# Optimization experiments

Hardware: AMD Instinct MI355X
Metric: run time of the kernel (lower is better)

## Reference

```python
import jax, jax.numpy as jnp
import numpy as np

N_NODES = 100000
N_EDGES = 1000000
N_GRAPHS = 2000
D = 64
BN_EPS = 1e-5


def setup_inputs() -> dict:
    key = jax.random.key(0)
    ks = jax.random.split(key, 16)
    x = jax.random.normal(ks[0], (N_NODES, D), dtype=jnp.float32)
    edge_index = jax.random.randint(ks[1], (2, N_EDGES), 0, N_NODES, dtype=jnp.int64)
    batch = jnp.sort(jax.random.randint(ks[2], (N_NODES,), 0, N_GRAPHS, dtype=jnp.int64))
    convW = jax.random.normal(ks[3], (3, D, D), dtype=jnp.float32) * 0.1
    convb = jax.random.normal(ks[4], (3, D), dtype=jnp.float32) * 0.1
    bn_gamma = jax.random.uniform(ks[5], (3, D), dtype=jnp.float32) + 0.5
    bn_beta = jax.random.normal(ks[6], (3, D), dtype=jnp.float32) * 0.1
    bn_mean = jax.random.normal(ks[7], (3, D), dtype=jnp.float32) * 0.1
    bn_var = jax.random.uniform(ks[8], (3, D), dtype=jnp.float32) + 0.5
    eps = jnp.zeros((3,), dtype=jnp.float32)
    clfW0 = jax.random.normal(ks[9], (256, 256), dtype=jnp.float32) * 0.05
    clfb0 = jax.random.normal(ks[10], (256,), dtype=jnp.float32) * 0.05
    clfW1 = jax.random.normal(ks[11], (256, 128), dtype=jnp.float32) * 0.05
    clfb1 = jax.random.normal(ks[12], (128,), dtype=jnp.float32) * 0.05
    finalW = jax.random.normal(ks[13], (128, 1), dtype=jnp.float32) * 0.05
    finalb = jnp.zeros((1,), dtype=jnp.float32)
    return {"x": x, "edge_index": edge_index, "batch": batch, "convW": convW,
            "convb": convb, "bn_gamma": bn_gamma, "bn_beta": bn_beta,
            "bn_mean": bn_mean, "bn_var": bn_var, "eps": eps,
            "clfW0": clfW0, "clfb0": clfb0, "clfW1": clfW1, "clfb1": clfb1,
            "finalW": finalW, "finalb": finalb}


def reference(x, edge_index, batch, convW, convb, bn_gamma, bn_beta, bn_mean,
              bn_var, eps, clfW0, clfb0, clfW1, clfb1, finalW, finalb):
    leaky = jax.nn.leaky_relu  # slope 0.01, matches torch default
    src, dst = edge_index[0], edge_index[1]
    n = x.shape[0]
    hs = []
    for l in range(3):
        # GINConv: (1 + eps) * x_i + sum_{j in N(i)} x_j  (scatter-add over edges)
        agg = jax.ops.segment_sum(x[src], dst, num_segments=n)
        h = (1.0 + eps[l]) * x + agg
        # MLP: Linear -> BatchNorm1d (eval, running stats) -> LeakyReLU (Dropout is identity in eval)
        h = h @ convW[l] + convb[l]
        h = (h - bn_mean[l]) * jax.lax.rsqrt(bn_var[l] + BN_EPS) * bn_gamma[l] + bn_beta[l]
        h = leaky(h)
        # extra LeakyReLU applied in GIN.forward after each conv layer
        h = leaky(h)
        x = h
        hs.append(h)
    # global_add_pool then repeat_interleave back to nodes (batch is sorted)
    h_pool = jax.ops.segment_sum(x, batch, num_segments=N_GRAPHS)
    h_pool_per_node = h_pool[batch]
    h = jnp.concatenate(hs + [h_pool_per_node], axis=1)  # [N, 256]
    h = leaky(h @ clfW0 + clfb0)
    h = leaky(h @ clfW1 + clfb1)
    h = h @ finalW + finalb
    return jax.nn.sigmoid(h)
```

## Files before the change

### kernel.cpp

```cpp
#include <hip/hip_runtime.h>

#define N_NODES 100000
#define PADM    100096
#define N_EDGES 1000000
#define N_GRAPHS 2000
#define D 64

typedef __bf16    bf16x8 __attribute__((ext_vector_type(8)));
typedef __bf16    bf16x4 __attribute__((ext_vector_type(4)));
typedef float     f32x4  __attribute__((ext_vector_type(4)));

__device__ __forceinline__ size_t apack(int row, int col, int fpr) {
  int frag = (row >> 4) * fpr + (col >> 5);
  int lane = (((col & 31) >> 3) << 4) | (row & 15);
  return (size_t)frag * 512 + lane * 8 + (col & 7);
}

__global__ __launch_bounds__(256) void deg_hist_kernel(
    const int* __restrict__ ei, int* __restrict__ deg)
{
  int i = blockIdx.x * blockDim.x + threadIdx.x;
  if (i < N_EDGES) atomicAdd(&deg[ei[N_EDGES + i]], 1);
}

__global__ __launch_bounds__(256) void scan1_kernel(
    const int* __restrict__ deg, int* __restrict__ incl, int* __restrict__ bsum)
{
  __shared__ int sh[256];
  int t = threadIdx.x;
  int base = blockIdx.x * 2048 + t * 8;
  int v[8];
  int run = 0;
#pragma unroll
  for (int j = 0; j < 8; ++j) {
    int idx = base + j;
    int xv = (idx < N_NODES) ? deg[idx] : 0;
    run += xv;
    v[j] = run;
  }
  sh[t] = run;
  __syncthreads();
  for (int off = 1; off < 256; off <<= 1) {
    int a = (t >= off) ? sh[t - off] : 0;
    __syncthreads();
    sh[t] += a;
    __syncthreads();
  }
  int prev = (t > 0) ? sh[t - 1] : 0;
#pragma unroll
  for (int j = 0; j < 8; ++j) {
    int idx = base + j;
    if (idx < N_NODES) incl[idx] = v[j] + prev;
  }
  if (t == 255) bsum[blockIdx.x] = sh[255];
}

__global__ void scan2_kernel(int* __restrict__ bsum, int nb)
{
  if (blockIdx.x == 0 && threadIdx.x == 0) {
    int run = 0;
    for (int i = 0; i < nb; ++i) { int xv = bsum[i]; bsum[i] = run; run += xv; }
  }
}

__global__ __launch_bounds__(256) void scan3_kernel(
    const int* __restrict__ incl, const int* __restrict__ bsum,
    const int* __restrict__ deg, int* __restrict__ row_ptr, int* __restrict__ cursor)
{
  int i = blockIdx.x * blockDim.x + threadIdx.x;
  if (i < N_NODES) {
    int val = incl[i] + bsum[i >> 11];
    row_ptr[i + 1] = val;
    cursor[i] = val - deg[i];
    if (i == 0) row_ptr[0] = 0;
  }
}

__global__ __launch_bounds__(256) void fill_csr_kernel(
    const int* __restrict__ ei, int* __restrict__ cursor, int* __restrict__ srcs)
{
  int i = blockIdx.x * blockDim.x + threadIdx.x;
  if (i < N_EDGES) {
    int s = ei[i];
    int d = ei[N_EDGES + i];
    int pos = atomicAdd(&cursor[d], 1);
    srcs[pos] = s;
  }
}

__global__ __launch_bounds__(256) void split_x_kernel(
    const float* __restrict__ x, __bf16* __restrict__ xhi, __bf16* __restrict__ xlo)
{
  int idx = blockIdx.x * blockDim.x + threadIdx.x;
  if (idx >= N_NODES * 16) return;
  int v = idx >> 4, c4 = (idx & 15) << 2;
  float4 xv = *(const float4*)(x + (size_t)v * D + c4);
  float p[4] = {xv.x, xv.y, xv.z, xv.w};
  bf16x4 vh, vl;
#pragma unroll
  for (int j = 0; j < 4; ++j) {
    __bf16 h = (__bf16)p[j];
    vh[j] = h;
    vl[j] = (__bf16)(p[j] - (float)h);
  }
  size_t o = apack(v, c4, 2);
  *(bf16x4*)(xhi + o) = vh;
  *(bf16x4*)(xlo + o) = vl;
}

__global__ __launch_bounds__(256) void wconv_kernel(
    const float* __restrict__ W0, const float* __restrict__ W1,
    const float* __restrict__ convW,
    __bf16* __restrict__ w0hi, __bf16* __restrict__ w0lo,
    __bf16* __restrict__ w1hi, __bf16* __restrict__ w1lo,
    __bf16* __restrict__ cwhi, __bf16* __restrict__ cwlo)
{
  int i = blockIdx.x * 256 + threadIdx.x;
  if (i < 65536) {
    int k = i >> 8, n = i & 255;
    float v = W0[i];
    __bf16 h = (__bf16)v;
    size_t o = apack(n, k, 8);
    w0hi[o] = h;
    w0lo[o] = (__bf16)(v - (float)h);
  }
  if (i < 32768) {
    int k = i >> 7, n = i & 127;
    float v = W1[i];
    __bf16 h = (__bf16)v;
    size_t o = apack(n, k, 8);
    w1hi[o] = h;
    w1lo[o] = (__bf16)(v - (float)h);
  }
  if (i < 12288) {
    int l = i >> 12, rem = i & 4095;
    int k = rem >> 6, n = rem & 63;
    float v = convW[i];
    __bf16 h = (__bf16)v;
    size_t o = (size_t)l * 4096 + apack(n, k, 2);
    cwhi[o] = h;
    cwlo[o] = (__bf16)(v - (float)h);
  }
}

__global__ __launch_bounds__(256) void ygemm_kernel(
    const __bf16* __restrict__ Ahi, const __bf16* __restrict__ Alo,
    int fpr, int fbase,
    const __bf16* __restrict__ cwh, const __bf16* __restrict__ cwl,
    float* __restrict__ y)
{
  int t = threadIdx.x;
  int wid = t >> 6, lane = t & 63;
  int bm0 = blockIdx.x * 64 + wid * 16;
  int rowtile = bm0 >> 4;
  int l15 = lane & 15;
  f32x4 acc[4];
#pragma unroll
  for (int j = 0; j < 4; ++j) acc[j] = (f32x4){0.f, 0.f, 0.f, 0.f};

#pragma unroll
  for (int kc = 0; kc < 2; ++kc) {
    bf16x8 ah, al, bh[4], bl[4];
    {
      size_t off = (size_t)(rowtile * fpr + fbase + kc) * 512 + lane * 8;
      ah = *(const bf16x8*)(Ahi + off);
      al = *(const bf16x8*)(Alo + off);
    }
#pragma unroll
    for (int ct = 0; ct < 4; ++ct) {
      size_t off = (size_t)(ct * 2 + kc) * 512 + lane * 8;
      bh[ct] = *(const bf16x8*)(cwh + off);
      bl[ct] = *(const bf16x8*)(cwl + off);
    }
#pragma unroll
    for (int ct = 0; ct < 4; ++ct) {
      acc[ct] = __builtin_amdgcn_mfma_f32_16x16x32_bf16(ah, bh[ct], acc[ct], 0, 0, 0);
      acc[ct] = __builtin_amdgcn_mfma_f32_16x16x32_bf16(al, bh[ct], acc[ct], 0, 0, 0);
      acc[ct] = __builtin_amdgcn_mfma_f32_16x16x32_bf16(ah, bl[ct], acc[ct], 0, 0, 0);
      acc[ct] = __builtin_amdgcn_mfma_f32_16x16x32_bf16(al, bl[ct], acc[ct], 0, 0, 0);
    }
  }
  int rbase = (lane >> 4) * 4;
#pragma unroll
  for (int ct = 0; ct < 4; ++ct)
#pragma unroll
    for (int r = 0; r < 4; ++r)
      y[(size_t)(bm0 + rbase + r) * D + 16 * ct + l15] = acc[ct][r];
}

template <int POOL>
__global__ __launch_bounds__(256) void agg_bn_kernel(
    const float* __restrict__ y,
    const int* __restrict__ row_ptr, const int* __restrict__ srcs,
    const float* __restrict__ bias,
    const float* __restrict__ gamma, const float* __restrict__ beta,
    const float* __restrict__ mean, const float* __restrict__ var,
    const float* __restrict__ epsp,
    __bf16* __restrict__ ohi, __bf16* __restrict__ olo, int oc0,
    float* __restrict__ hpool, const int* __restrict__ batch)
{
  int wid = (blockIdx.x * blockDim.x + threadIdx.x) >> 6;
  int lane = threadIdx.x & 63;
  if (wid >= N_NODES) return;
  float onepe = 1.0f + epsp[0];
  int beg = row_ptr[wid];
  int end = row_ptr[wid + 1];
  float s = onepe * y[(size_t)wid * D + lane];
  int e = beg;
  for (; e + 8 <= end; e += 8) {
    int i0 = srcs[e], i1 = srcs[e + 1], i2 = srcs[e + 2], i3 = srcs[e + 3];
    int i4 = srcs[e + 4], i5 = srcs[e + 5], i6 = srcs[e + 6], i7 = srcs[e + 7];
    float a0 = y[(size_t)i0 * D + lane];
    float a1 = y[(size_t)i1 * D + lane];
    float a2 = y[(size_t)i2 * D + lane];
    float a3 = y[(size_t)i3 * D + lane];
    float a4 = y[(size_t)i4 * D + lane];
    float a5 = y[(size_t)i5 * D + lane];
    float a6 = y[(size_t)i6 * D + lane];
    float a7 = y[(size_t)i7 * D + lane];
    s += ((a0 + a1) + (a2 + a3)) + ((a4 + a5) + (a6 + a7));
  }
  for (; e + 4 <= end; e += 4) {
    int i0 = srcs[e], i1 = srcs[e + 1], i2 = srcs[e + 2], i3 = srcs[e + 3];
    float a0 = y[(size_t)i0 * D + lane];
    float a1 = y[(size_t)i1 * D + lane];
    float a2 = y[(size_t)i2 * D + lane];
    float a3 = y[(size_t)i3 * D + lane];
    s += (a0 + a1) + (a2 + a3);
  }
  for (; e < end; ++e) s += y[(size_t)srcs[e] * D + lane];

  float sc = gamma[lane] * rsqrtf(var[lane] + 1e-5f);
  float z = (s + bias[lane] - mean[lane]) * sc + beta[lane];
  z = (z > 0.f) ? z : 0.01f * z;
  z = (z > 0.f) ? z : 0.01f * z;
  __bf16 h = (__bf16)z;
  size_t o = apack(wid, oc0 + lane, 8);
  ohi[o] = h;
  olo[o] = (__bf16)(z - (float)h);
  if (POOL) {
    int g = batch[wid];
    unsafeAtomicAdd(&hpool[(size_t)g * D + lane], z);
  }
}

__global__ __launch_bounds__(256) void pool_expand_kernel(
    const float* __restrict__ hpool, const int* __restrict__ batch,
    __bf16* __restrict__ ohi, __bf16* __restrict__ olo)
{
  int idx = blockIdx.x * blockDim.x + threadIdx.x;
  int v = idx >> 4, c4 = (idx & 15) << 2;
  if (v >= N_NODES) return;
  int g = batch[v];
  float4 pv = *(const float4*)(hpool + (size_t)g * D + c4);
  float p[4] = {pv.x, pv.y, pv.z, pv.w};
  bf16x4 vh, vl;
#pragma unroll
  for (int j = 0; j < 4; ++j) {
    __bf16 h = (__bf16)p[j];
    vh[j] = h;
    vl[j] = (__bf16)(p[j] - (float)h);
  }
  size_t o = apack(v, 192 + c4, 8);
  *(bf16x4*)(ohi + o) = vh;
  *(bf16x4*)(olo + o) = vl;
}

__global__ __launch_bounds__(256) void clf_fused_kernel(
    const __bf16* __restrict__ Ahi, const __bf16* __restrict__ Alo,
    const __bf16* __restrict__ w0h, const __bf16* __restrict__ w0l,
    const float* __restrict__ b0,
    const __bf16* __restrict__ w1h, const __bf16* __restrict__ w1l,
    const float* __restrict__ b1,
    const float* __restrict__ Wf, const float* __restrict__ fbias,
    float* __restrict__ out)
{
  __shared__ __bf16 HaS[64 * 128];
  __shared__ __bf16 LaS[64 * 128];
  int t = threadIdx.x;
  int w = t >> 6, lane = t & 63;
  int wr = w >> 1, wc = w & 1;
  int l15 = lane & 15, g = lane >> 4, lk = g * 8;
  int bm0 = blockIdx.x * 64;
  int rtile0 = (bm0 >> 4) + 2 * wr;

  f32x4 acc2[2][4];
#pragma unroll
  for (int i = 0; i < 2; ++i)
#pragma unroll
    for (int j = 0; j < 4; ++j) acc2[i][j] = (f32x4){0.f, 0.f, 0.f, 0.f};

  for (int h = 0; h < 2; ++h) {
    f32x4 acc[2][4];
#pragma unroll
    for (int i = 0; i < 2; ++i)
#pragma unroll
      for (int j = 0; j < 4; ++j) acc[i][j] = (f32x4){0.f, 0.f, 0.f, 0.f};

    int ntile0 = 8 * h + 4 * wc;
    for (int ks = 0; ks < 8; ++ks) {
      bf16x8 ah[2], al[2], bh[4], bl[4];
#pragma unroll
      for (int rt = 0; rt < 2; ++rt) {
        size_t off = (size_t)((rtile0 + rt) * 8 + ks) * 512 + lane * 8;
        ah[rt] = *(const bf16x8*)(Ahi + off);
        al[rt] = *(const bf16x8*)(Alo + off);
      }
#pragma unroll
      for (int ct = 0; ct < 4; ++ct) {
        size_t off = (size_t)((ntile0 + ct) * 8 + ks) * 512 + lane * 8;
        bh[ct] = *(const bf16x8*)(w0h + off);
        bl[ct] = *(const bf16x8*)(w0l + off);
      }
#pragma unroll
      for (int rt = 0; rt < 2; ++rt)
#pragma unroll
        for (int ct = 0; ct < 4; ++ct) {
          acc[rt][ct] = __builtin_amdgcn_mfma_f32_16x16x32_bf16(ah[rt], bh[ct], acc[rt][ct], 0, 0, 0);
          acc[rt][ct] = __builtin_amdgcn_mfma_f32_16x16x32_bf16(al[rt], bh[ct], acc[rt][ct], 0, 0, 0);
          acc[rt][ct] = __builtin_amdgcn_mfma_f32_16x16x32_bf16(ah[rt], bl[ct], acc[rt][ct], 0, 0, 0);
        }
    }
#pragma unroll
    for (int rt = 0; rt < 2; ++rt)
#pragma unroll
      for (int ct = 0; ct < 4; ++ct) {
        int coll = 64 * wc + 16 * ct + l15;
        float bb = b0[128 * h + coll];
#pragma unroll
        for (int r = 0; r < 4; ++r) {
          int rowl = 32 * wr + 16 * rt + 4 * g + r;
          float z = acc[rt][ct][r] + bb;
          z = (z > 0.f) ? z : 0.01f * z;
          __bf16 hv = (__bf16)z;
          unsigned bo = (unsigned)(rowl * 256 + coll * 2) ^ ((rowl & 7) << 4);
          *(__bf16*)((char*)HaS + bo) = hv;
          *(__bf16*)((char*)LaS + bo) = (__bf16)(z - (float)hv);
        }
      }
    __syncthreads();

    for (int ks = 0; ks < 4; ++ks) {
      int kl = ks * 32;
      bf16x8 ah2[2], al2[2], b2h[4], b2l[4];
#pragma unroll
      for (int rt = 0; rt < 2; ++rt) {
        int rowl = 32 * wr + 16 * rt + l15;
        unsigned bo = (unsigned)(rowl * 256 + (kl + lk) * 2) ^ ((rowl & 7) << 4);
        ah2[rt] = *(const bf16x8*)((char*)HaS + bo);
        al2[rt] = *(const bf16x8*)((char*)LaS + bo);
      }
#pragma unroll
      for (int ct = 0; ct < 4; ++ct) {
        size_t off = (size_t)((4 * wc + ct) * 8 + 4 * h + ks) * 512 + lane * 8;
        b2h[ct] = *(const bf16x8*)(w1h + off);
        b2l[ct] = *(const bf16x8*)(w1l + off);
      }
#pragma unroll
      for (int rt = 0; rt < 2; ++rt)
#pragma unroll
        for (int ct = 0; ct < 4; ++ct) {
          acc2[rt][ct] = __builtin_amdgcn_mfma_f32_16x16x32_bf16(ah2[rt], b2h[ct], acc2[rt][ct], 0, 0, 0);
          acc2[rt][ct] = __builtin_amdgcn_mfma_f32_16x16x32_bf16(al2[rt], b2h[ct], acc2[rt][ct], 0, 0, 0);
          acc2[rt][ct] = __builtin_amdgcn_mfma_f32_16x16x32_bf16(ah2[rt], b2l[ct], acc2[rt][ct], 0, 0, 0);
        }
    }
    __syncthreads();
  }

  float* partS = (float*)HaS;
#pragma unroll
  for (int rt = 0; rt < 2; ++rt) {
#pragma unroll
    for (int r = 0; r < 4; ++r) {
      int rowl = 32 * wr + 16 * rt + 4 * g + r;
      float p = 0.f;
#pragma unroll
      for (int ct = 0; ct < 4; ++ct) {
        int c = 64 * wc + 16 * ct + l15;
        float z = acc2[rt][ct][r] + b1[c];
        z = (z > 0.f) ? z : 0.01f * z;
        p += z * Wf[c];
      }
      p += __shfl_xor(p, 1);
      p += __shfl_xor(p, 2);
      p += __shfl_xor(p, 4);
      p += __shfl_xor(p, 8);
      if (l15 == 0) partS[wc * 64 + rowl] = p;
    }
  }
  __syncthreads();
  if (t < 64) {
    int gl = bm0 + t;
    if (gl < N_NODES) {
      float z = partS[t] + partS[64 + t] + fbias[0];
      out[gl] = 1.0f / (1.0f + expf(-z));
    }
  }
}

extern "C" void kernel_launch(void* const* d_in, const int* in_sizes, int n_in,
                              void* d_out, int out_size, void* d_ws, size_t ws_size,
                              hipStream_t stream)
{
  const float* x     = (const float*)d_in[0];
  const int*   ei    = (const int*)d_in[1];
  const int*   batch = (const int*)d_in[2];
  const float* convW = (const float*)d_in[3];
  const float* convb = (const float*)d_in[4];
  const float* gam   = (const float*)d_in[5];
  const float* bet   = (const float*)d_in[6];
  const float* mean  = (const float*)d_in[7];
  const float* var   = (const float*)d_in[8];
  const float* eps   = (const float*)d_in[9];
  const float* W0    = (const float*)d_in[10];
  const float* b0    = (const float*)d_in[11];
  const float* W1    = (const float*)d_in[12];
  const float* b1    = (const float*)d_in[13];
  const float* Wf    = (const float*)d_in[14];
  const float* fb    = (const float*)d_in[15];
  float* out = (float*)d_out;

  float* ws = (float*)d_ws;
  __bf16* A0hi = (__bf16*)(ws);
  __bf16* A0lo = (__bf16*)(ws + 12812288);
  float*  y    = ws + 25624576;
  __bf16* xhi  = (__bf16*)(ws + 32030720);
  __bf16* xlo  = (__bf16*)(ws + 35230720);
  int* deg     = (int*)(ws + 38436864);
  int* incl    = (int*)(ws + 38536864);
  int* row_ptr = (int*)(ws + 38636864);
  int* cursor  = (int*)(ws + 38736896);
  int* srcs    = (int*)(ws + 38836896);
  int* bsum    = (int*)(ws + 39836896);
  float* hpool = ws + 39836960;
  __bf16* w0hi = (__bf16*)(ws + 39964960);
  __bf16* w0lo = (__bf16*)(ws + 39997728);
  __bf16* w1hi = (__bf16*)(ws + 40030496);
  __bf16* w1lo = (__bf16*)(ws + 40046880);
  __bf16* cwhi = (__bf16*)(ws + 40063264);
  __bf16* cwlo = (__bf16*)(ws + 40069408);

  dim3 b256(256);

  wconv_kernel<<<256, b256, 0, stream>>>(W0, W1, convW, w0hi, w0lo, w1hi, w1lo, cwhi, cwlo);

  hipMemsetAsync(deg, 0, (size_t)N_NODES * sizeof(int), stream);
  deg_hist_kernel<<<(N_EDGES + 255) / 256, b256, 0, stream>>>(ei, deg);
  scan1_kernel<<<(N_NODES + 2047) / 2048, b256, 0, stream>>>(deg, incl, bsum);
  scan2_kernel<<<1, 64, 0, stream>>>(bsum, (N_NODES + 2047) / 2048);
  scan3_kernel<<<(N_NODES + 255) / 256, b256, 0, stream>>>(incl, bsum, deg, row_ptr, cursor);
  fill_csr_kernel<<<(N_EDGES + 255) / 256, b256, 0, stream>>>(ei, cursor, srcs);

  hipMemsetAsync(hpool, 0, (size_t)N_GRAPHS * D * sizeof(float), stream);
  split_x_kernel<<<(N_NODES * 16 + 255) / 256, b256, 0, stream>>>(x, xhi, xlo);

  int ygrid = PADM / 64;
  int aggGrid = (N_NODES * 64 + 255) / 256;

  ygemm_kernel<<<ygrid, b256, 0, stream>>>(xhi, xlo, 2, 0, cwhi, cwlo, y);
  agg_bn_kernel<0><<<aggGrid, b256, 0, stream>>>(
      y, row_ptr, srcs, convb, gam, bet, mean, var, eps, A0hi, A0lo, 0, nullptr, nullptr);
  ygemm_kernel<<<ygrid, b256, 0, stream>>>(A0hi, A0lo, 8, 0, cwhi + 4096, cwlo + 4096, y);
  agg_bn_kernel<0><<<aggGrid, b256, 0, stream>>>(
      y, row_ptr, srcs, convb + D, gam + D, bet + D, mean + D, var + D, eps + 1,
      A0hi, A0lo, 64, nullptr, nullptr);
  ygemm_kernel<<<ygrid, b256, 0, stream>>>(A0hi, A0lo, 8, 2, cwhi + 8192, cwlo + 8192, y);
  agg_bn_kernel<1><<<aggGrid, b256, 0, stream>>>(
      y, row_ptr, srcs, convb + 2 * D, gam + 2 * D, bet + 2 * D, mean + 2 * D,
      var + 2 * D, eps + 2, A0hi, A0lo, 128, hpool, batch);

  pool_expand_kernel<<<(N_NODES * 16 + 255) / 256, b256, 0, stream>>>(hpool, batch, A0hi, A0lo);

  clf_fused_kernel<<<PADM / 64, b256, 0, stream>>>(
      A0hi, A0lo, w0hi, w0lo, b0, w1hi, w1lo, b1, Wf, fb, out);
}
```

Measured before the change: 438.3 us.

## Process four nodes per wave with float4 gathers in aggregation kernel

```diff
diff --git a/kernel.cpp b/kernel.cpp
--- a/kernel.cpp
+++ b/kernel.cpp
@@ -199,48 +199,67 @@
     __bf16* __restrict__ ohi, __bf16* __restrict__ olo, int oc0,
     float* __restrict__ hpool, const int* __restrict__ batch)
 {
-  int wid = (blockIdx.x * blockDim.x + threadIdx.x) >> 6;
+  int wave = (blockIdx.x * blockDim.x + threadIdx.x) >> 6;
   int lane = threadIdx.x & 63;
-  if (wid >= N_NODES) return;
+  int sub = lane >> 4;
+  int sl  = lane & 15;
+  int node = wave * 4 + sub;
+  if (node >= N_NODES) return;
   float onepe = 1.0f + epsp[0];
-  int beg = row_ptr[wid];
-  int end = row_ptr[wid + 1];
-  float s = onepe * y[(size_t)wid * D + lane];
+  int beg = row_ptr[node];
+  int end = row_ptr[node + 1];
+  const float4* yv = (const float4*)y;
+  float4 own = yv[(size_t)node * 16 + sl];
+  float4 s = make_float4(onepe * own.x, onepe * own.y, onepe * own.z, onepe * own.w);
   int e = beg;
-  for (; e + 8 <= end; e += 8) {
-    int i0 = srcs[e], i1 = srcs[e + 1], i2 = srcs[e + 2], i3 = srcs[e + 3];
-    int i4 = srcs[e + 4], i5 = srcs[e + 5], i6 = srcs[e + 6], i7 = srcs[e + 7];
-    float a0 = y[(size_t)i0 * D + lane];
-    float a1 = y[(size_t)i1 * D + lane];
-    float a2 = y[(size_t)i2 * D + lane];
-    float a3 = y[(size_t)i3 * D + lane];
-    float a4 = y[(size_t)i4 * D + lane];
-    float a5 = y[(size_t)i5 * D + lane];
-    float a6 = y[(size_t)i6 * D + lane];
-    float a7 = y[(size_t)i7 * D + lane];
-    s += ((a0 + a1) + (a2 + a3)) + ((a4 + a5) + (a6 + a7));
-  }
   for (; e + 4 <= end; e += 4) {
     int i0 = srcs[e], i1 = srcs[e + 1], i2 = srcs[e + 2], i3 = srcs[e + 3];
-    float a0 = y[(size_t)i0 * D + lane];
-    float a1 = y[(size_t)i1 * D + lane];
-    float a2 = y[(size_t)i2 * D + lane];
-    float a3 = y[(size_t)i3 * D + lane];
-    s += (a0 + a1) + (a2 + a3);
-  }
-  for (; e < end; ++e) s += y[(size_t)srcs[e] * D + lane];
-
-  float sc = gamma[lane] * rsqrtf(var[lane] + 1e-5f);
-  float z = (s + bias[lane] - mean[lane]) * sc + beta[lane];
-  z = (z > 0.f) ? z : 0.01f * z;
-  z = (z > 0.f) ? z : 0.01f * z;
-  __bf16 h = (__bf16)z;
-  size_t o = apack(wid, oc0 + lane, 8);
-  ohi[o] = h;
-  olo[o] = (__bf16)(z - (float)h);
+    float4 a0 = yv[(size_t)i0 * 16 + sl];
+    float4 a1 = yv[(size_t)i1 * 16 + sl];
+    float4 a2 = yv[(size_t)i2 * 16 + sl];
+    float4 a3 = yv[(size_t)i3 * 16 + sl];
+    s.x += (a0.x + a1.x) + (a2.x + a3.x);
+    s.y += (a0.y + a1.y) + (a2.y + a3.y);
+    s.z += (a0.z + a1.z) + (a2.z + a3.z);
+    s.w += (a0.w + a1.w) + (a2.w + a3.w);
+  }
+  for (; e < end; ++e) {
+    float4 a = yv[(size_t)srcs[e] * 16 + sl];
+    s.x += a.x; s.y += a.y; s.z += a.z; s.w += a.w;
+  }
+
+  float4 gv = *(const float4*)(gamma + sl * 4);
+  float4 vv = *(const float4*)(var + sl * 4);
+  float4 bv = *(const float4*)(bias + sl * 4);
+  float4 mv = *(const float4*)(mean + sl * 4);
+  float4 tv = *(const float4*)(beta + sl * 4);
+  float sm[4] = {s.x, s.y, s.z, s.w};
+  float gg[4] = {gv.x, gv.y, gv.z, gv.w};
+  float va[4] = {vv.x, vv.y, vv.z, vv.w};
+  float bb[4] = {bv.x, bv.y, bv.z, bv.w};
+  float mm[4] = {mv.x, mv.y, mv.z, mv.w};
+  float tt[4] = {tv.x, tv.y, tv.z, tv.w};
+  bf16x4 vh, vl;
+  float zz[4];
+#pragma unroll
+  for (int j = 0; j < 4; ++j) {
+    float sc = gg[j] * rsqrtf(va[j] + 1e-5f);
+    float z = (sm[j] + bb[j] - mm[j]) * sc + tt[j];
+    z = (z > 0.f) ? z : 0.01f * z;
+    z = (z > 0.f) ? z : 0.01f * z;
+    zz[j] = z;
+    __bf16 h = (__bf16)z;
+    vh[j] = h;
+    vl[j] = (__bf16)(z - (float)h);
+  }
+  size_t o = apack(node, oc0 + sl * 4, 8);
+  *(bf16x4*)(ohi + o) = vh;
+  *(bf16x4*)(olo + o) = vl;
   if (POOL) {
-    int g = batch[wid];
-    unsafeAtomicAdd(&hpool[(size_t)g * D + lane], z);
+    int g = batch[node];
+#pragma unroll
+    for (int j = 0; j < 4; ++j)
+      unsafeAtomicAdd(&hpool[(size_t)g * D + sl * 4 + j], zz[j]);
   }
 }
 
@@ -456,7 +475,7 @@
   split_x_kernel<<<(N_NODES * 16 + 255) / 256, b256, 0, stream>>>(x, xhi, xlo);
 
   int ygrid = PADM / 64;
-  int aggGrid = (N_NODES * 64 + 255) / 256;
+  int aggGrid = (N_NODES + 15) / 16;
 
   ygemm_kernel<<<ygrid, b256, 0, stream>>>(xhi, xlo, 2, 0, cwhi, cwlo, y);
   agg_bn_kernel<0><<<aggGrid, b256, 0, stream>>>(
```

New measurement: 487.5 us. 1.11x slower.

## Store GEMM output in column-sliced layout and aggregate per 8-column slice

Applied to the files above, without the earlier changes.

```diff
diff --git a/kernel.cpp b/kernel.cpp
--- a/kernel.cpp
+++ b/kernel.cpp
@@ -147,7 +147,7 @@
     const __bf16* __restrict__ Ahi, const __bf16* __restrict__ Alo,
     int fpr, int fbase,
     const __bf16* __restrict__ cwh, const __bf16* __restrict__ cwl,
-    float* __restrict__ y)
+    float* __restrict__ ysl)
 {
   int t = threadIdx.x;
   int wid = t >> 6, lane = t & 63;
@@ -184,13 +184,16 @@
 #pragma unroll
   for (int ct = 0; ct < 4; ++ct)
 #pragma unroll
-    for (int r = 0; r < 4; ++r)
-      y[(size_t)(bm0 + rbase + r) * D + 16 * ct + l15] = acc[ct][r];
+    for (int r = 0; r < 4; ++r) {
+      int col = 16 * ct + l15;
+      int node = bm0 + rbase + r;
+      ysl[(size_t)(col >> 3) * (PADM * 8) + (size_t)node * 8 + (col & 7)] = acc[ct][r];
+    }
 }
 
 template <int POOL>
 __global__ __launch_bounds__(256) void agg_bn_kernel(
-    const float* __restrict__ y,
+    const float* __restrict__ ysl,
     const int* __restrict__ row_ptr, const int* __restrict__ srcs,
     const float* __restrict__ bias,
     const float* __restrict__ gamma, const float* __restrict__ beta,
@@ -199,48 +202,44 @@
     __bf16* __restrict__ ohi, __bf16* __restrict__ olo, int oc0,
     float* __restrict__ hpool, const int* __restrict__ batch)
 {
-  int wid = (blockIdx.x * blockDim.x + threadIdx.x) >> 6;
+  int slice = blockIdx.x & 7;
+  int nb = blockIdx.x >> 3;
+  int w = threadIdx.x >> 6;
   int lane = threadIdx.x & 63;
-  if (wid >= N_NODES) return;
+  int e8 = lane >> 3, c = lane & 7;
+  const float* ys = ysl + (size_t)slice * (PADM * 8);
+  int cb = slice * 8 + c;
   float onepe = 1.0f + epsp[0];
-  int beg = row_ptr[wid];
-  int end = row_ptr[wid + 1];
-  float s = onepe * y[(size_t)wid * D + lane];
-  int e = beg;
-  for (; e + 8 <= end; e += 8) {
-    int i0 = srcs[e], i1 = srcs[e + 1], i2 = srcs[e + 2], i3 = srcs[e + 3];
-    int i4 = srcs[e + 4], i5 = srcs[e + 5], i6 = srcs[e + 6], i7 = srcs[e + 7];
-    float a0 = y[(size_t)i0 * D + lane];
-    float a1 = y[(size_t)i1 * D + lane];
-    float a2 = y[(size_t)i2 * D + lane];
-    float a3 = y[(size_t)i3 * D + lane];
-    float a4 = y[(size_t)i4 * D + lane];
-    float a5 = y[(size_t)i5 * D + lane];
-    float a6 = y[(size_t)i6 * D + lane];
-    float a7 = y[(size_t)i7 * D + lane];
-    s += ((a0 + a1) + (a2 + a3)) + ((a4 + a5) + (a6 + a7));
-  }
-  for (; e + 4 <= end; e += 4) {
-    int i0 = srcs[e], i1 = srcs[e + 1], i2 = srcs[e + 2], i3 = srcs[e + 3];
-    float a0 = y[(size_t)i0 * D + lane];
-    float a1 = y[(size_t)i1 * D + lane];
-    float a2 = y[(size_t)i2 * D + lane];
-    float a3 = y[(size_t)i3 * D + lane];
-    s += (a0 + a1) + (a2 + a3);
-  }
-  for (; e < end; ++e) s += y[(size_t)srcs[e] * D + lane];
-
-  float sc = gamma[lane] * rsqrtf(var[lane] + 1e-5f);
-  float z = (s + bias[lane] - mean[lane]) * sc + beta[lane];
-  z = (z > 0.f) ? z : 0.01f * z;
-  z = (z > 0.f) ? z : 0.01f * z;
-  __bf16 h = (__bf16)z;
-  size_t o = apack(wid, oc0 + lane, 8);
-  ohi[o] = h;
-  olo[o] = (__bf16)(z - (float)h);
-  if (POOL) {
-    int g = batch[wid];
-    unsafeAtomicAdd(&hpool[(size_t)g * D + lane], z);
+  float sc = gamma[cb] * rsqrtf(var[cb] + 1e-5f);
+  float bb = bias[cb], mm = mean[cb], tt = beta[cb];
+  int n0 = nb * 64 + w * 16;
+#pragma unroll 1
+  for (int i = 0; i < 16; ++i) {
+    int n = n0 + i;
+    if (n >= N_NODES) break;
+    int beg = row_ptr[n], end = row_ptr[n + 1];
+    float s = 0.f;
+    for (int e0 = beg; e0 < end; e0 += 8) {
+      int e = e0 + e8;
+      float v = 0.f;
+      if (e < end) v = ys[(size_t)srcs[e] * 8 + c];
+      s += v;
+    }
+    s += __shfl_xor(s, 8);
+    s += __shfl_xor(s, 16);
+    s += __shfl_xor(s, 32);
+    float own = ys[(size_t)n * 8 + c];
+    float z = (onepe * own + s + bb - mm) * sc + tt;
+    z = (z > 0.f) ? z : 0.01f * z;
+    z = (z > 0.f) ? z : 0.01f * z;
+    if (e8 == 0) {
+      __bf16 h = (__bf16)z;
+      size_t o = apack(n, oc0 + cb, 8);
+      ohi[o] = h;
+      olo[o] = (__bf16)(z - (float)h);
+      if (POOL)
+        unsafeAtomicAdd(&hpool[(size_t)batch[n] * D + cb], z);
+    }
   }
 }
 
@@ -456,7 +455,7 @@
   split_x_kernel<<<(N_NODES * 16 + 255) / 256, b256, 0, stream>>>(x, xhi, xlo);
 
   int ygrid = PADM / 64;
-  int aggGrid = (N_NODES * 64 + 255) / 256;
+  int aggGrid = ((N_NODES + 63) / 64) * 8;
 
   ygemm_kernel<<<ygrid, b256, 0, stream>>>(xhi, xlo, 2, 0, cwhi, cwlo, y);
   agg_bn_kernel<0><<<aggGrid, b256, 0, stream>>>(
```

Result: slower. 853.2 us (+94.7%).
